# Optimization experiments

Hardware: AMD Instinct MI355X
Metric: run time of the kernel (lower is better)

## Reference

```python
import jax, jax.numpy as jnp
import numpy as np

NUM_CLASSES = 80
STRIDES = (8, 16, 32)
PRE_TOP_K = 1000
KEEP_TOP_K = 100
IOU_THR = 0.65
SCORE_THR = 0.25
CLASS_OFFSET = 8192.0  # > max image coordinate, separates classes for batched NMS


def _make_priors_strides(featmap_sizes):
    # MlvlPointGenerator.grid_priors with offset=0 (RTMDet-style point priors)
    priors, strides = [], []
    for (h, w), s in zip(featmap_sizes, STRIDES):
        ys, xs = jnp.meshgrid(jnp.arange(h, dtype=jnp.float32) * s,
                              jnp.arange(w, dtype=jnp.float32) * s, indexing='ij')
        priors.append(jnp.stack([xs.reshape(-1), ys.reshape(-1)], axis=-1))
        strides.append(jnp.full((h * w,), float(s), dtype=jnp.float32))
    return jnp.concatenate(priors, 0), jnp.concatenate(strides, 0)


def _flatten(x, c):
    # [B, C, H, W] -> [B, H*W, c] matching permute(0,2,3,1).reshape
    b = x.shape[0]
    return jnp.transpose(x, (0, 2, 3, 1)).reshape(b, -1, c)


def _iou_matrix(boxes):
    # boxes [K, 4] x1y1x2y2 -> pairwise IoU [K, K]
    area = jnp.maximum(boxes[:, 2] - boxes[:, 0], 0.0) * jnp.maximum(boxes[:, 3] - boxes[:, 1], 0.0)
    lt = jnp.maximum(boxes[:, None, :2], boxes[None, :, :2])
    rb = jnp.minimum(boxes[:, None, 2:], boxes[None, :, 2:])
    wh = jnp.maximum(rb - lt, 0.0)
    inter = wh[..., 0] * wh[..., 1]
    return inter / jnp.maximum(area[:, None] + area[None, :] - inter, 1e-6)


def _nms_single(boxes, scores, labels):
    # boxes [N,4], scores [N] (max over classes), labels [N] int32
    valid = scores > SCORE_THR
    scores = jnp.where(valid, scores, 0.0)
    top_scores, idx = jax.lax.top_k(scores, PRE_TOP_K)  # pre_top_k filtering
    b = boxes[idx]
    lab = labels[idx]
    val = valid[idx]
    # class-aware NMS via coordinate offset per class (batched_nms trick)
    off_boxes = b + (lab.astype(b.dtype) * CLASS_OFFSET)[:, None]
    iou = _iou_matrix(off_boxes)

    def body(suppressed, i):
        keep_i = ~suppressed[i]
        suppressed = suppressed | (keep_i & (iou[i] > IOU_THR))
        suppressed = suppressed.at[i].set(~keep_i)
        return suppressed, keep_i

    _, keeps = jax.lax.scan(body, ~val, jnp.arange(PRE_TOP_K))
    final_scores = jnp.where(keeps, top_scores, 0.0)
    fs, fidx = jax.lax.top_k(final_scores, KEEP_TOP_K)
    dets = jnp.concatenate([b[fidx], fs[:, None]], axis=-1)  # [keep_top_k, 5]
    return dets, lab[fidx]


def setup_inputs() -> dict:
    key = jax.random.key(0)
    ks = jax.random.split(key, 6)
    B, C = 16, NUM_CLASSES
    return {
        'cls0': jax.random.normal(ks[0], (B, C, 80, 80), jnp.float32),
        'cls1': jax.random.normal(ks[1], (B, C, 40, 40), jnp.float32),
        'cls2': jax.random.normal(ks[2], (B, C, 20, 20), jnp.float32),
        'box0': jax.random.uniform(ks[3], (B, 4, 80, 80), jnp.float32),
        'box1': jax.random.uniform(ks[4], (B, 4, 40, 40), jnp.float32),
        'box2': jax.random.uniform(ks[5], (B, 4, 20, 20), jnp.float32),
    }


def reference(cls0, cls1, cls2, box0, box1, box2):
    featmap_sizes = [c.shape[2:] for c in (cls0, cls1, cls2)]
    priors, strides = _make_priors_strides(featmap_sizes)  # [A,2], [A]
    scores = jax.nn.sigmoid(
        jnp.concatenate([_flatten(c, NUM_CLASSES) for c in (cls0, cls1, cls2)], axis=1))  # [B,A,C]
    preds = jnp.concatenate([_flatten(b, 4) for b in (box0, box1, box2)], axis=1)  # [B,A,4]
    # rtmdet_bbox_decoder: distances * stride around point priors
    d = preds * strides[None, :, None]
    x1 = priors[None, :, 0] - d[..., 0]
    y1 = priors[None, :, 1] - d[..., 1]
    x2 = priors[None, :, 0] + d[..., 2]
    y2 = priors[None, :, 1] + d[..., 3]
    bboxes = jnp.stack([x1, y1, x2, y2], axis=-1)  # [B,A,4]
    max_scores = jnp.max(scores, axis=-1)
    labels = jnp.argmax(scores, axis=-1).astype(jnp.int32)
    dets, out_labels = jax.vmap(_nms_single)(bboxes, max_scores, labels)
    return dets, out_labels
```

## Files before the change

kernel.cpp:

```cpp
#include <hip/hip_runtime.h>
#include <math.h>
#include <stdint.h>

typedef unsigned long long u64;
typedef unsigned int u32;

#define NCLS 80
#define NA   8400
#define NB   16
#define PRE_K 1000
#define M_FAST 256
#define CHUNKS 17
#define MAGIC  0x13579BDF2468ACE1ull


__global__ __launch_bounds__(1024) void k_fused(
    const float* __restrict__ cls0, const float* __restrict__ cls1,
    const float* __restrict__ cls2, const float* __restrict__ box0,
    const float* __restrict__ box1, const float* __restrict__ box2,
    u64* __restrict__ f_keys, float4* __restrict__ boxes,
    u64* __restrict__ flags, float* __restrict__ out)
{
    __shared__ __align__(16) char shm[65536];
    __shared__ __align__(16) u64 cbs[1024];
    __shared__ u32 wtot[16];
    __shared__ u32 s_total, s_B, s_kept;
    int tid = threadIdx.x, lane = tid & 63, wv = tid >> 6;
    int b = blockIdx.y;

    if (blockIdx.x != 0) {
        int c  = blockIdx.x - 1;
        int t  = tid & 255;
        int q  = tid >> 8;
        int pa = c * 256 + t;
        bool act = pa < 4200;

        float* pm0 = (float*)shm;
        float* pm1 = (float*)(shm + 3072);
        int*   pl0 = (int*)(shm + 6144);
        int*   pl1 = (int*)(shm + 9216);

        const float *clsp = cls0, *boxp = box0;
        int Wd = 80, ss = 8, HW = 6400, hw = 0;
        float m0 = -1e30f, m1 = -1e30f;
        int lab0 = q * 20, lab1 = q * 20;

        if (act) {
            if (pa < 3200)      { clsp = cls0; boxp = box0; Wd = 80; ss = 8;  HW = 6400; hw = 2 * pa; }
            else if (pa < 4000) { clsp = cls1; boxp = box1; Wd = 40; ss = 16; HW = 1600; hw = 2 * pa - 6400; }
            else                { clsp = cls2; boxp = box2; Wd = 20; ss = 32; HW = 400;  hw = 2 * pa - 8000; }

            const float* cp = clsp + (size_t)b * NCLS * HW + (size_t)(q * 20) * HW + hw;
            float2 v = *(const float2*)cp;
            m0 = v.x; m1 = v.y;
#pragma unroll 5
            for (int c2 = 1; c2 < 20; ++c2) {
                float2 vv = *(const float2*)(cp + (size_t)c2 * HW);
                if (vv.x > m0) { m0 = vv.x; lab0 = q * 20 + c2; }
                if (vv.y > m1) { m1 = vv.y; lab1 = q * 20 + c2; }
            }
            if (q > 0) {
                pm0[(q - 1) * 256 + t] = m0; pl0[(q - 1) * 256 + t] = lab0;
                pm1[(q - 1) * 256 + t] = m1; pl1[(q - 1) * 256 + t] = lab1;
            }
        }
        __syncthreads();
        if (act) {
            int a = 2 * pa;
            if (q == 0) {
#pragma unroll
                for (int k = 0; k < 3; ++k) {
                    float a0 = pm0[k * 256 + t]; if (a0 > m0) { m0 = a0; lab0 = pl0[k * 256 + t]; }
                    float a1 = pm1[k * 256 + t]; if (a1 > m1) { m1 = a1; lab1 = pl1[k * 256 + t]; }
                }
                double e0 = exp(-(double)m0), e1 = exp(-(double)m1);
                float sc0 = (float)(1.0 / (1.0 + e0));
                float sc1 = (float)(1.0 / (1.0 + e1));
                float sz0 = (sc0 > 0.25f) ? sc0 : 0.0f;
                float sz1 = (sc1 > 0.25f) ? sc1 : 0.0f;
                u32 lo0 = ~(((u32)a << 7) | (u32)lab0);
                u32 lo1 = ~((((u32)(a + 1)) << 7) | (u32)lab1);
                u64* fkp = f_keys + (size_t)b * NA + a;
                fkp[0] = ((u64)__float_as_uint(sz0) << 32) | (u64)lo0;
                fkp[1] = ((u64)__float_as_uint(sz1) << 32) | (u64)lo1;
            } else if (q == 1) {
                const float* bp = boxp + (size_t)b * 4 * HW + hw;
                float fs = (float)ss;
                float2 q0v = *(const float2*)(bp);
                float2 q1v = *(const float2*)(bp + HW);
                float2 q2v = *(const float2*)(bp + 2 * HW);
                float2 q3v = *(const float2*)(bp + 3 * HW);
                float px = (float)((hw % Wd) * ss);
                float py = (float)((hw / Wd) * ss);
                float px1 = px + fs;
                boxes[(size_t)b * NA + a]     = make_float4(px  - q0v.x * fs, py - q1v.x * fs, px  + q2v.x * fs, py + q3v.x * fs);
                boxes[(size_t)b * NA + a + 1] = make_float4(px1 - q0v.y * fs, py - q1v.y * fs, px1 + q2v.y * fs, py + q3v.y * fs);
            }
        }
        __syncthreads();
        if (tid == 0) {
            __threadfence();
            __hip_atomic_store(&flags[b * CHUNKS + c], MAGIC,
                               __ATOMIC_RELAXED, __HIP_MEMORY_SCOPE_AGENT);
        }
        return;
    }

    if (tid == 0) {
        for (int i = 0; i < CHUNKS; ++i) {
            while (__hip_atomic_load(&flags[b * CHUNKS + i],
                                     __ATOMIC_RELAXED, __HIP_MEMORY_SCOPE_AGENT) != MAGIC)
                __builtin_amdgcn_s_sleep(8);
        }
        __threadfence();
    }
    __syncthreads();

    const u64* fk = f_keys + (size_t)b * NA;

    u64 kr[9];
#pragma unroll
    for (int k = 0; k < 9; ++k) {
        int i = tid + k * 1024;
        kr[k] = (i < NA) ? fk[i] : 0ull;
    }

    {
        u32* R  = (u32*)shm;
        u32* C  = (u32*)(shm + 16384);
        u64* BK = (u64*)(shm + 32768);

        for (int i = tid; i < 4096; i += 1024) { R[i] = 0; C[i] = 0; }
        __syncthreads();

#pragma unroll
        for (int k = 0; k < 9; ++k) {
            u32 sb = (u32)(kr[k] >> 32);
            if (sb) {
                int bin = (int)(sb >> 12) - 0x3E800;
                bin = max(0, min(bin, 4095));
                atomicAdd(&R[bin], 1u);
            }
        }
        __syncthreads();

        u32 h0 = R[4*tid], h1 = R[4*tid+1], h2 = R[4*tid+2], h3 = R[4*tid+3];
        u32 g = h0 + h1 + h2 + h3;
        u32 S = g;
#pragma unroll
        for (int off = 1; off < 64; off <<= 1) {
            u32 x = __shfl_down(S, off, 64);
            if (lane + off < 64) S += x;
        }
        if (lane == 0) wtot[wv] = S;
        __syncthreads();
        u32 wsuf = 0;
#pragma unroll
        for (int w = 0; w < 16; ++w) if (w > wv) wsuf += wtot[w];
        u32 above = (S - g) + wsuf;
        u32 r3 = h3 + above, r2 = h2 + r3, r1 = h1 + r2, r0 = h0 + r1;
        R[4*tid] = r0; R[4*tid+1] = r1; R[4*tid+2] = r2; R[4*tid+3] = r3;
        if (tid == 0) s_total = 0;
        __syncthreads();
        if (tid == 0) s_total = R[0];
        __syncthreads();
        u32 total = s_total;

        if (tid == 0 && total < PRE_K) s_B = 0;
#pragma unroll
        for (int k = 0; k < 4; ++k) {
            int bin = 4*tid + k;
            u32 Rb = R[bin];
            u32 Rn = (bin < 4095) ? R[bin + 1] : 0;
            if (Rb >= PRE_K && Rn < PRE_K) s_B = (u32)bin;
        }
        __syncthreads();
        u32 B = s_B;
        u32 Cv = R[B];

        if (Cv <= 4096) {
#pragma unroll
            for (int k = 0; k < 9; ++k) {
                u64 key = kr[k];
                u32 sb = (u32)(key >> 32);
                if (sb) {
                    int bin = (int)(sb >> 12) - 0x3E800;
                    bin = max(0, min(bin, 4095));
                    if ((u32)bin >= B) {
                        u32 base = (bin < 4095) ? R[bin + 1] : 0;
                        u32 off = atomicAdd(&C[bin], 1u);
                        BK[base + off] = key;
                    }
                }
            }
            __syncthreads();
            for (int s2 = tid; s2 < (int)Cv; s2 += 1024) {
                u64 key = BK[s2];
                u32 sb = (u32)(key >> 32);
                int bin = (int)(sb >> 12) - 0x3E800;
                bin = max(0, min(bin, 4095));
                u32 base = (bin < 4095) ? R[bin + 1] : 0;
                u32 n = R[bin] - base;
                u32 cnt = 0;
                for (u32 j = 0; j < n; ++j) cnt += (BK[base + j] > key) ? 1u : 0u;
                u32 rank = base + cnt;
                if (rank < PRE_K) cbs[rank] = key;
            }
        } else {
            for (int i = tid; i < NA; i += 1024) {
                u64 key = fk[i];
                u32 sb = (u32)(key >> 32);
                if (!sb) continue;
                int bin = (int)(sb >> 12) - 0x3E800;
                bin = max(0, min(bin, 4095));
                if ((u32)bin < B) continue;
                u32 rank = 0;
                for (int j = 0; j < NA; ++j) rank += (fk[j] > key) ? 1u : 0u;
                if (rank < PRE_K) cbs[rank] = key;
            }
        }
        for (int t2 = tid; (int)total + t2 < PRE_K; t2 += 1024)
            cbs[total + t2] = (u64)(u32)~((u32)t2 << 7);
        __syncthreads();
    }

    float4* sbox = (float4*)shm;
    float*  sar  = (float*)(shm + 16384);
    u64*    mk   = (u64*)(shm + 20480);
    u64*    Ksh  = (u64*)(shm + 28672);
    int*    chgA = (int*)(shm + 28928);

    if (tid < M_FAST) {
        u64 key = cbs[tid];
        u32 v = ~(u32)key;
        u32 a = v >> 7;
        float4 bx = boxes[(size_t)b * NA + a];
        float off = (float)(v & 127u) * 8192.0f;
        float x1 = bx.x + off, y1 = bx.y + off, x2 = bx.z + off, y2 = bx.w + off;
        sbox[tid] = make_float4(x1, y1, x2, y2);
        float w = fmaxf(__fsub_rn(x2, x1), 0.0f);
        float h = fmaxf(__fsub_rn(y2, y1), 0.0f);
        sar[tid] = __fmul_rn(w, h);
    }
    __syncthreads();

    {
        int i = tid & 255, w = tid >> 8;
        u64 bits = 0;
        int iw = i >> 6;
        if (w <= iw) {
            int jmax = (w < iw) ? 64 : (i & 63);
            float4 A = sbox[i];
            float aar = sar[i];
            const float4* bj = sbox + w * 64;
            const float*  aj = sar  + w * 64;
            for (int jj = 0; jj < jmax; ++jj) {
                float4 Bx = bj[jj];
                float sab = aj[jj];
                float lx = fmaxf(A.x, Bx.x), ly = fmaxf(A.y, Bx.y);
                float rx = fminf(A.z, Bx.z), ry = fminf(A.w, Bx.w);
                float ww = fmaxf(__fsub_rn(rx, lx), 0.0f);
                float hh = fmaxf(__fsub_rn(ry, ly), 0.0f);
                float inter = __fmul_rn(ww, hh);
                float uni = __fsub_rn(__fadd_rn(aar, sab), inter);
                if (inter > 0.65f * fmaxf(uni, 1e-6f)) bits |= (1ull << jj);
            }
        }
        mk[i * 4 + w] = bits;
    }
    __syncthreads();

    bool inr = tid < M_FAST;
    u64 key = (tid < PRE_K) ? cbs[tid] : 0ull;
    bool valid = inr && ((u32)(key >> 32) != 0u);
    u64 rowm4[4];
#pragma unroll
    for (int k = 0; k < 4; ++k) rowm4[k] = inr ? mk[tid * 4 + k] : 0ull;

    u64 v0 = __ballot(valid);
    if (inr && lane == 0) Ksh[wv] = v0;
    if (tid < 32) chgA[tid] = 0;
    __syncthreads();

    int fin = 0;
    for (int it = 0; it < M_FAST + 2; ++it) {
        int p = it & 1;
        const u64* Kc = Ksh + p * 4;
        u64 kold = inr ? Kc[wv] : 0ull;
        u64 acc = 0;
#pragma unroll
        for (int k = 0; k < 4; ++k) acc |= rowm4[k] & Kc[k];
        bool kept = valid && (acc == 0ull);
        u64 nk = __ballot(kept);
        if (inr && lane == 0) {
            Ksh[(p ^ 1) * 4 + wv] = nk;
            if (nk != kold) chgA[it & 31] = 1;
        }
        __syncthreads();
        fin = p ^ 1;
        if (chgA[it & 31] == 0) break;
        if ((it & 31) == 31) {
            __syncthreads();
            if (tid < 32) chgA[tid] = 0;
            __syncthreads();
        }
    }
    const u64* Kf = Ksh + fin * 4;
    if (tid == 0) {
        u32 kt = 0;
#pragma unroll
        for (int k = 0; k < 4; ++k) kt += __popcll(Kf[k]);
        s_kept = kt;
    }
    __syncthreads();

    if (s_kept >= 100) {
        if (inr) {
            bool kept = (Kf[wv] >> lane) & 1ull;
            u64 low = (1ull << lane) - 1ull;
            int pc = 0;
#pragma unroll
            for (int k = 0; k < 4; ++k) {
                u64 lt = (k < wv) ? ~0ull : ((k == wv) ? low : 0ull);
                pc += __popcll(Kf[k] & lt);
            }
            if (kept && pc < 100) {
                u32 v = ~(u32)key;
                u32 a = v >> 7;
                float4 bx = boxes[(size_t)b * NA + a];
                float fsc = __uint_as_float((u32)(key >> 32));
                float* dr = out + (size_t)(b * 100 + pc) * 5;
                dr[0] = bx.x; dr[1] = bx.y; dr[2] = bx.z; dr[3] = bx.w; dr[4] = fsc;
                out[(size_t)NB * 100 * 5 + b * 100 + pc] = (float)(v & 127u);
            }
        }
        return;
    }

    {
        if (tid >= M_FAST && tid < PRE_K) {
            u64 kk = cbs[tid];
            u32 v = ~(u32)kk;
            u32 a = v >> 7;
            float4 bx = boxes[(size_t)b * NA + a];
            float off = (float)(v & 127u) * 8192.0f;
            float x1 = bx.x + off, y1 = bx.y + off, x2 = bx.z + off, y2 = bx.w + off;
            sbox[tid] = make_float4(x1, y1, x2, y2);
            float w = fmaxf(__fsub_rn(x2, x1), 0.0f);
            float h = fmaxf(__fsub_rn(y2, y1), 0.0f);
            sar[tid] = __fmul_rn(w, h);
        }
        __syncthreads();

        bool inrF = tid < PRE_K;
        u64 rowm[16];
#pragma unroll
        for (int k = 0; k < 16; ++k) rowm[k] = 0ull;
        if (inrF) {
            float4 A = sbox[tid];
            float aar = sar[tid];
            for (int k = 0; k <= wv; ++k) {
                int jmax = (k < wv) ? 64 : lane;
                const float4* bj = sbox + k * 64;
                const float*  aj = sar  + k * 64;
                u64 bits = 0;
                for (int jj = 0; jj < jmax; ++jj) {
                    float4 Bx = bj[jj];
                    float sab = aj[jj];
                    float lx = fmaxf(A.x, Bx.x), ly = fmaxf(A.y, Bx.y);
                    float rx = fminf(A.z, Bx.z), ry = fminf(A.w, Bx.w);
                    float ww = fmaxf(__fsub_rn(rx, lx), 0.0f);
                    float hh = fmaxf(__fsub_rn(ry, ly), 0.0f);
                    float inter = __fmul_rn(ww, hh);
                    float uni = __fsub_rn(__fadd_rn(aar, sab), inter);
                    if (inter > 0.65f * fmaxf(uni, 1e-6f)) bits |= (1ull << jj);
                }
                rowm[k] = bits;
            }
        }
        bool valid2 = inrF && ((u32)(key >> 32) != 0u);

        u64 vF = __ballot(valid2);
        if (lane == 0) Ksh[wv] = vF;
        if (tid < 32) chgA[tid] = 0;
        __syncthreads();

        int finF = 0;
        for (int it = 0; it < PRE_K + 2; ++it) {
            int p = it & 1;
            const u64* Kc = Ksh + p * 16;
            u64 kold = Kc[wv];
            u64 acc = 0;
#pragma unroll
            for (int k = 0; k < 16; ++k) acc |= rowm[k] & Kc[k];
            bool kept = valid2 && (acc == 0ull);
            u64 nk = __ballot(kept);
            if (lane == 0) {
                Ksh[(p ^ 1) * 16 + wv] = nk;
                if (nk != kold) chgA[it & 31] = 1;
            }
            __syncthreads();
            finF = p ^ 1;
            if (chgA[it & 31] == 0) break;
            if ((it & 31) == 31) {
                __syncthreads();
                if (tid < 32) chgA[tid] = 0;
                __syncthreads();
            }
        }
        const u64* Kf2 = Ksh + finF * 16;

        u64 low = (1ull << lane) - 1ull;
        int pc = 0, Kt = 0;
#pragma unroll
        for (int k = 0; k < 16; ++k) {
            u64 kk = Kf2[k];
            u64 lt = (k < wv) ? ~0ull : ((k == wv) ? low : 0ull);
            pc += __popcll(kk & lt);
            Kt += __popcll(kk);
        }
        if (inrF) {
            bool kept = (Kf2[wv] >> lane) & 1ull;
            int row = kept ? pc : (Kt + (tid - pc));
            if (row < 100) {
                u32 v = ~(u32)key;
                u32 a = v >> 7;
                float4 bx = boxes[(size_t)b * NA + a];
                float fsc = kept ? __uint_as_float((u32)(key >> 32)) : 0.0f;
                float* dr = out + (size_t)(b * 100 + row) * 5;
                dr[0] = bx.x; dr[1] = bx.y; dr[2] = bx.z; dr[3] = bx.w; dr[4] = fsc;
                out[(size_t)NB * 100 * 5 + b * 100 + row] = (float)(v & 127u);
            }
        }
    }
}

extern "C" void kernel_launch(void* const* d_in, const int* in_sizes, int n_in,
                              void* d_out, int out_size, void* d_ws, size_t ws_size,
                              hipStream_t stream) {
    const float* cls0 = (const float*)d_in[0];
    const float* cls1 = (const float*)d_in[1];
    const float* cls2 = (const float*)d_in[2];
    const float* box0 = (const float*)d_in[3];
    const float* box1 = (const float*)d_in[4];
    const float* box2 = (const float*)d_in[5];
    float* out = (float*)d_out;

    char* w = (char*)d_ws;
    u64*    f_keys = (u64*)(w);
    float4* boxes  = (float4*)(w + 1075200);
    u64*    flags  = (u64*)(w + 3225600);

    k_fused<<<dim3(1 + CHUNKS, NB), 1024, 0, stream>>>(
        cls0, cls1, cls2, box0, box1, box2, f_keys, boxes, flags, out);
}
```

Baseline: 117.0 us.

## Split fused kernel into separate decode and NMS kernels, drop flag spin-wait

Replaces the single fused kernel, where one block per image spin-waited on global flags set by producer blocks, with two launches: a decode kernel using 256-thread blocks and float4 loads over four anchors per thread, and a post-processing kernel per image. The kernel boundary replaces the atomic flag handshake and fence. This removes the spin-wait and the stale-flag hazard and widens decode parallelism, at the cost of an extra kernel launch and losing the overlap of the waiting block.

```diff
diff --git a/kernel.cpp b/kernel.cpp
--- a/kernel.cpp
+++ b/kernel.cpp
@@ -10,111 +10,107 @@
 #define NB   16
 #define PRE_K 1000
 #define M_FAST 256
-#define CHUNKS 17
-#define MAGIC  0x13579BDF2468ACE1ull
-
-
-__global__ __launch_bounds__(1024) void k_fused(
+
+
+__global__ __launch_bounds__(256) void k_decode(
     const float* __restrict__ cls0, const float* __restrict__ cls1,
     const float* __restrict__ cls2, const float* __restrict__ box0,
     const float* __restrict__ box1, const float* __restrict__ box2,
-    u64* __restrict__ f_keys, float4* __restrict__ boxes,
-    u64* __restrict__ flags, float* __restrict__ out)
+    u64* __restrict__ f_keys, float4* __restrict__ boxes)
+{
+    __shared__ float4 pmx[3][64];
+    __shared__ int4   plb[3][64];
+
+    int l  = threadIdx.x & 63;
+    int w  = threadIdx.x >> 6;
+    int b  = blockIdx.y;
+    int a0 = blockIdx.x * 256 + 4 * l;
+    bool act = a0 < NA;
+
+    const float *clsp = cls0, *boxp = box0;
+    int Wd = 80, ss = 8, HW = 6400, hw0 = 0;
+    if (act) {
+        if (a0 < 6400)      { clsp = cls0; boxp = box0; Wd = 80; ss = 8;  HW = 6400; hw0 = a0; }
+        else if (a0 < 8000) { clsp = cls1; boxp = box1; Wd = 40; ss = 16; HW = 1600; hw0 = a0 - 6400; }
+        else                { clsp = cls2; boxp = box2; Wd = 20; ss = 32; HW = 400;  hw0 = a0 - 8000; }
+    }
+
+    float4 mx = make_float4(-1e30f, -1e30f, -1e30f, -1e30f);
+    int4   lb = make_int4(w * 20, w * 20, w * 20, w * 20);
+
+    if (act) {
+        const float* cp = clsp + (size_t)b * NCLS * HW + (size_t)(w * 20) * HW + hw0;
+        mx = *(const float4*)cp;
+#pragma unroll
+        for (int c = 1; c < 20; ++c) {
+            float4 v = *(const float4*)(cp + (size_t)c * HW);
+            if (v.x > mx.x) { mx.x = v.x; lb.x = w * 20 + c; }
+            if (v.y > mx.y) { mx.y = v.y; lb.y = w * 20 + c; }
+            if (v.z > mx.z) { mx.z = v.z; lb.z = w * 20 + c; }
+            if (v.w > mx.w) { mx.w = v.w; lb.w = w * 20 + c; }
+        }
+        if (w > 0) { pmx[w - 1][l] = mx; plb[w - 1][l] = lb; }
+    }
+    __syncthreads();
+    if (!act) return;
+
+    if (w == 0) {
+#pragma unroll
+        for (int k = 0; k < 3; ++k) {
+            float4 o = pmx[k][l]; int4 ol = plb[k][l];
+            if (o.x > mx.x) { mx.x = o.x; lb.x = ol.x; }
+            if (o.y > mx.y) { mx.y = o.y; lb.y = ol.y; }
+            if (o.z > mx.z) { mx.z = o.z; lb.z = ol.z; }
+            if (o.w > mx.w) { mx.w = o.w; lb.w = ol.w; }
+        }
+        float mv[4] = {mx.x, mx.y, mx.z, mx.w};
+        int   lv[4] = {lb.x, lb.y, lb.z, lb.w};
+        u64 kk[4];
+#pragma unroll
+        for (int j = 0; j < 4; ++j) {
+            double e = exp(-(double)mv[j]);
+            float sc = (float)(1.0 / (1.0 + e));
+            float sz = (sc > 0.25f) ? sc : 0.0f;
+            u32 lo = ~((((u32)(a0 + j)) << 7) | (u32)lv[j]);
+            kk[j] = ((u64)__float_as_uint(sz) << 32) | (u64)lo;
+        }
+        u64* fkp = f_keys + (size_t)b * NA + a0;
+        *(ulonglong2*)(fkp)     = make_ulonglong2(kk[0], kk[1]);
+        *(ulonglong2*)(fkp + 2) = make_ulonglong2(kk[2], kk[3]);
+    } else if (w == 1) {
+        const float* bp = boxp + (size_t)b * 4 * HW + hw0;
+        float fs = (float)ss;
+        float4 d0 = *(const float4*)(bp);
+        float4 d1 = *(const float4*)(bp + HW);
+        float4 d2 = *(const float4*)(bp + 2 * HW);
+        float4 d3 = *(const float4*)(bp + 3 * HW);
+        int qx = hw0 % Wd, qy = hw0 / Wd;
+        float4* bo = boxes + (size_t)b * NA + a0;
+        float l0[4] = {d0.x, d0.y, d0.z, d0.w};
+        float t0[4] = {d1.x, d1.y, d1.z, d1.w};
+        float r0[4] = {d2.x, d2.y, d2.z, d2.w};
+        float b0[4] = {d3.x, d3.y, d3.z, d3.w};
+#pragma unroll
+        for (int j = 0; j < 4; ++j) {
+            float px = (float)(qx * ss);
+            float py = (float)(qy * ss);
+            bo[j] = make_float4(px - l0[j] * fs, py - t0[j] * fs,
+                                px + r0[j] * fs, py + b0[j] * fs);
+            ++qx; if (qx == Wd) { qx = 0; ++qy; }
+        }
+    }
+}
+
+__global__ __launch_bounds__(1024, 1) void k_post(
+    const u64* __restrict__ f_keys, const float4* __restrict__ boxes,
+    float* __restrict__ out)
 {
     __shared__ __align__(16) char shm[65536];
     __shared__ __align__(16) u64 cbs[1024];
     __shared__ u32 wtot[16];
     __shared__ u32 s_total, s_B, s_kept;
     int tid = threadIdx.x, lane = tid & 63, wv = tid >> 6;
-    int b = blockIdx.y;
-
-    if (blockIdx.x != 0) {
-        int c  = blockIdx.x - 1;
-        int t  = tid & 255;
-        int q  = tid >> 8;
-        int pa = c * 256 + t;
-        bool act = pa < 4200;
-
-        float* pm0 = (float*)shm;
-        float* pm1 = (float*)(shm + 3072);
-        int*   pl0 = (int*)(shm + 6144);
-        int*   pl1 = (int*)(shm + 9216);
-
-        const float *clsp = cls0, *boxp = box0;
-        int Wd = 80, ss = 8, HW = 6400, hw = 0;
-        float m0 = -1e30f, m1 = -1e30f;
-        int lab0 = q * 20, lab1 = q * 20;
-
-        if (act) {
-            if (pa < 3200)      { clsp = cls0; boxp = box0; Wd = 80; ss = 8;  HW = 6400; hw = 2 * pa; }
-            else if (pa < 4000) { clsp = cls1; boxp = box1; Wd = 40; ss = 16; HW = 1600; hw = 2 * pa - 6400; }
-            else                { clsp = cls2; boxp = box2; Wd = 20; ss = 32; HW = 400;  hw = 2 * pa - 8000; }
-
-            const float* cp = clsp + (size_t)b * NCLS * HW + (size_t)(q * 20) * HW + hw;
-            float2 v = *(const float2*)cp;
-            m0 = v.x; m1 = v.y;
-#pragma unroll 5
-            for (int c2 = 1; c2 < 20; ++c2) {
-                float2 vv = *(const float2*)(cp + (size_t)c2 * HW);
-                if (vv.x > m0) { m0 = vv.x; lab0 = q * 20 + c2; }
-                if (vv.y > m1) { m1 = vv.y; lab1 = q * 20 + c2; }
-            }
-            if (q > 0) {
-                pm0[(q - 1) * 256 + t] = m0; pl0[(q - 1) * 256 + t] = lab0;
-                pm1[(q - 1) * 256 + t] = m1; pl1[(q - 1) * 256 + t] = lab1;
-            }
-        }
-        __syncthreads();
-        if (act) {
-            int a = 2 * pa;
-            if (q == 0) {
-#pragma unroll
-                for (int k = 0; k < 3; ++k) {
-                    float a0 = pm0[k * 256 + t]; if (a0 > m0) { m0 = a0; lab0 = pl0[k * 256 + t]; }
-                    float a1 = pm1[k * 256 + t]; if (a1 > m1) { m1 = a1; lab1 = pl1[k * 256 + t]; }
-                }
-                double e0 = exp(-(double)m0), e1 = exp(-(double)m1);
-                float sc0 = (float)(1.0 / (1.0 + e0));
-                float sc1 = (float)(1.0 / (1.0 + e1));
-                float sz0 = (sc0 > 0.25f) ? sc0 : 0.0f;
-                float sz1 = (sc1 > 0.25f) ? sc1 : 0.0f;
-                u32 lo0 = ~(((u32)a << 7) | (u32)lab0);
-                u32 lo1 = ~((((u32)(a + 1)) << 7) | (u32)lab1);
-                u64* fkp = f_keys + (size_t)b * NA + a;
-                fkp[0] = ((u64)__float_as_uint(sz0) << 32) | (u64)lo0;
-                fkp[1] = ((u64)__float_as_uint(sz1) << 32) | (u64)lo1;
-            } else if (q == 1) {
-                const float* bp = boxp + (size_t)b * 4 * HW + hw;
-                float fs = (float)ss;
-                float2 q0v = *(const float2*)(bp);
-                float2 q1v = *(const float2*)(bp + HW);
-                float2 q2v = *(const float2*)(bp + 2 * HW);
-                float2 q3v = *(const float2*)(bp + 3 * HW);
-                float px = (float)((hw % Wd) * ss);
-                float py = (float)((hw / Wd) * ss);
-                float px1 = px + fs;
-                boxes[(size_t)b * NA + a]     = make_float4(px  - q0v.x * fs, py - q1v.x * fs, px  + q2v.x * fs, py + q3v.x * fs);
-                boxes[(size_t)b * NA + a + 1] = make_float4(px1 - q0v.y * fs, py - q1v.y * fs, px1 + q2v.y * fs, py + q3v.y * fs);
-            }
-        }
-        __syncthreads();
-        if (tid == 0) {
-            __threadfence();
-            __hip_atomic_store(&flags[b * CHUNKS + c], MAGIC,
-                               __ATOMIC_RELAXED, __HIP_MEMORY_SCOPE_AGENT);
-        }
-        return;
-    }
-
-    if (tid == 0) {
-        for (int i = 0; i < CHUNKS; ++i) {
-            while (__hip_atomic_load(&flags[b * CHUNKS + i],
-                                     __ATOMIC_RELAXED, __HIP_MEMORY_SCOPE_AGENT) != MAGIC)
-                __builtin_amdgcn_s_sleep(8);
-        }
-        __threadfence();
-    }
-    __syncthreads();
+    int b = blockIdx.x;
 
     const u64* fk = f_keys + (size_t)b * NA;
 
@@ -449,8 +445,8 @@
     char* w = (char*)d_ws;
     u64*    f_keys = (u64*)(w);
     float4* boxes  = (float4*)(w + 1075200);
-    u64*    flags  = (u64*)(w + 3225600);
-
-    k_fused<<<dim3(1 + CHUNKS, NB), 1024, 0, stream>>>(
-        cls0, cls1, cls2, box0, box1, box2, f_keys, boxes, flags, out);
+
+    k_decode<<<dim3(33, NB), 256, 0, stream>>>(cls0, cls1, cls2, box0, box1, box2,
+                                               f_keys, boxes);
+    k_post<<<NB, 1024, 0, stream>>>(f_keys, boxes, out);
 }
```

Result: faster. 105.2 us (-10.1%).
